# Optimization experiments

Hardware: AMD Instinct MI355X
Metric: run time of the kernel (lower is better)

Reference implementation:

```python
import jax, jax.numpy as jnp
import numpy as np

EMBED_DIM = 64
NUM_CODES = 4096
BETA = 0.25  # commitment_cost


def setup_inputs() -> dict:
    key = jax.random.key(0)
    k1, k2 = jax.random.split(key)
    inputs = jax.random.normal(k1, (512, 8192, 1), dtype=jnp.float32)
    # tf.random_uniform_initializer default range [0, 0.05)
    embeddings = jax.random.uniform(k2, (EMBED_DIM, NUM_CODES), dtype=jnp.float32, minval=0.0, maxval=0.05)
    return {"inputs": inputs, "embeddings": embeddings}


def reference(inputs, embeddings):
    # MuModel.call, training=False (no EMA state updates at inference)
    x = inputs[:, :, 0]                       # [B, T]
    flat = x.reshape(-1, EMBED_DIM)           # [N, D]
    # squared L2 distances to each code: ||z||^2 - 2 z.E + ||e||^2  -> [N, K]
    distances = (
        jnp.sum(flat * flat, axis=1, keepdims=True)
        - 2.0 * (flat @ embeddings)
        + jnp.sum(embeddings * embeddings, axis=0, keepdims=True)
    )
    # tf uses argmax(-distances) == argmin(distances)
    idx = jnp.argmax(-distances, axis=1)      # [N] int
    # one-hot @ embeddings.T is just a gather of code vectors
    quantized = jnp.take(embeddings.T, idx, axis=0)   # [N, D]
    quantized = quantized.reshape(x.shape)            # [B, T]
    commitment_loss = BETA * jnp.mean((jax.lax.stop_gradient(quantized) - x) ** 2)
    quantized = x + jax.lax.stop_gradient(quantized - x)  # straight-through
    out = quantized[..., None]                # [B, T, 1]
    return (out, commitment_loss, idx)
```

## Files before the change

kernel.cpp:

```cpp
#include <hip/hip_runtime.h>
#include <float.h>

#define EMBED   64
#define CODES   4096
#define NROWS   65536
#define NELEM   4194304
#define BR      128
#define CCH     128
#define NCH     32
#define CUNITS  2048
#define NTILE   128

typedef __attribute__((ext_vector_type(8)))  short bf16x8;
typedef __attribute__((ext_vector_type(16))) float f32x16;

__device__ inline unsigned short f2bf(float f) {
    unsigned u = __float_as_uint(f);
    u += 0x7fff + ((u >> 16) & 1);
    return (unsigned short)(u >> 16);
}
__device__ inline float bf2f(unsigned short h) {
    return __uint_as_float(((unsigned)h) << 16);
}

__global__ void vq_setup(const float* __restrict__ E, float* __restrict__ cbuf,
                         double* __restrict__ accum, bf16x8* __restrict__ packed,
                         float* __restrict__ ET) {
    const int b = blockIdx.x, t = threadIdx.x;
    if (b < 16) {
        int j = b * 256 + t;
        float v = E[j];
        float s = __fmul_rn(v, v);
        for (int i = 1; i < EMBED; ++i) {
            v = E[(size_t)i * CODES + j];
            s = __fadd_rn(s, __fmul_rn(v, v));
        }
        cbuf[j] = s;
        if (j == 0) *accum = 0.0;
    } else if (b < 144) {
        int id = (b - 16) * 256 + t;
        int lam = id & 63, kk = (id >> 6) & 3, g = id >> 8;
        int n  = g * 32 + (lam & 31);
        int kb = kk * 16 + (lam >> 5) * 8;
        bf16x8 vh, vl;
#pragma unroll
        for (int j = 0; j < 8; ++j) {
            float e = E[(size_t)(kb + j) * CODES + n];
            unsigned short hi = f2bf(e);
            vh[j] = (short)hi;
            vl[j] = (short)f2bf(e - bf2f(hi));
        }
        packed[((g * 4 + kk) * 2 + 0) * 64 + lam] = vh;
        packed[((g * 4 + kk) * 2 + 1) * 64 + lam] = vl;
    } else {
        int id = (b - 144) * 256 + t;
        int j = id >> 4, i0 = (id & 15) * 4;
        float4 v;
        v.x = E[(size_t)(i0 + 0) * CODES + j];
        v.y = E[(size_t)(i0 + 1) * CODES + j];
        v.z = E[(size_t)(i0 + 2) * CODES + j];
        v.w = E[(size_t)(i0 + 3) * CODES + j];
        *(float4*)(ET + (size_t)j * EMBED + i0) = v;
    }
}

template <bool PRE>
__global__ __launch_bounds__(256, 2)
void vq_main(const float* __restrict__ X, const float* __restrict__ E,
             const float* __restrict__ cbuf, const bf16x8* __restrict__ packed,
             const float* __restrict__ ET, double* __restrict__ accum,
             float* __restrict__ out) {
    __shared__ bf16x8 lbuf[2][CUNITS];

    const int t  = threadIdx.x;
    const int l  = t & 63, wv = t >> 6;
    const int m  = l & 31, h  = l >> 5;
    const int row0 = blockIdx.x * BR;

    bf16x8 ah[4], al[4];
    float sqreg;
    {
        const float* xrow = X + (size_t)(row0 + wv * 32 + m) * EMBED;
        float sq = 0.f;
#pragma unroll
        for (int kk = 0; kk < 4; ++kk) {
            int kb = kk * 16 + h * 8;
            float4 v0 = *(const float4*)(xrow + kb);
            float4 v1 = *(const float4*)(xrow + kb + 4);
            float xv[8] = {v0.x, v0.y, v0.z, v0.w, v1.x, v1.y, v1.z, v1.w};
#pragma unroll
            for (int j = 0; j < 8; ++j) {
                sq = fmaf(xv[j], xv[j], sq);
                unsigned short hi = f2bf(xv[j]);
                float r = xv[j] - bf2f(hi);
                ah[kk][j] = (short)hi;
                al[kk][j] = (short)f2bf(r);
            }
        }
        sq += __shfl_xor(sq, 32, 64);
        sqreg = sq;
    }

    float M1[16], M2[16];
#pragma unroll
    for (int e = 0; e < 16; ++e) { M1[e] = -FLT_MAX; M2[e] = -FLT_MAX; }

    auto epi = [&](const f32x16& a, int g) {
        unsigned gu = (unsigned)g;
#pragma unroll
        for (int e = 0; e < 16; ++e) {
            float ap = __uint_as_float((__float_as_uint(a[e]) & 0xFFFFFF80u) | gu);
            float m1o = M1[e];
            M1[e] = fmaxf(m1o, ap);
            M2[e] = __builtin_amdgcn_fmed3f(m1o, M2[e], ap);
        }
    };

    if constexpr (PRE) {
        auto stage = [&](int ch, int buf) {
#pragma unroll
            for (int q = 0; q < 8; ++q) {
                const bf16x8* gp = packed + (size_t)ch * CUNITS + q * 256 + t;
                bf16x8* lp = &lbuf[buf][q * 256 + wv * 64];
                __builtin_amdgcn_global_load_lds(
                    (const __attribute__((address_space(1))) void*)gp,
                    (__attribute__((address_space(3))) void*)lp, 16, 0, 0);
            }
        };

        f32x16 pA, pB; int pGA = 0, pGB = 0;
#pragma unroll
        for (int e = 0; e < 16; ++e) { pA[e] = -FLT_MAX; pB[e] = -FLT_MAX; }

        const int ch0 = blockIdx.x & (NCH - 1);
        stage(ch0, 0);
        __syncthreads();

        int b = 0;
#pragma unroll 1
        for (int cc = 0; cc < NCH; ++cc) {
            int ch = ch0 + cc; if (ch >= NCH) ch -= NCH;
            if (cc + 1 < NCH) { int cn = ch + 1; if (cn >= NCH) cn -= NCH; stage(cn, b ^ 1); }
            const bf16x8* lb = lbuf[b];
#pragma unroll
            for (int pp = 0; pp < 2; ++pp) {
                const int tl0 = pp * 2, tl1 = tl0 + 1;
                const int g0 = ch * 4 + tl0, g1 = ch * 4 + tl1;
                bf16x8 B0[8], B1[8];
#pragma unroll
                for (int kk = 0; kk < 4; ++kk) {
                    B0[kk * 2]     = lb[tl0 * 512 + kk * 128 + l];
                    B0[kk * 2 + 1] = lb[tl0 * 512 + kk * 128 + 64 + l];
                    B1[kk * 2]     = lb[tl1 * 512 + kk * 128 + l];
                    B1[kk * 2 + 1] = lb[tl1 * 512 + kk * 128 + 64 + l];
                }
                float nc0 = -0.5f * cbuf[g0 * 32 + m];
                float nc1 = -0.5f * cbuf[g1 * 32 + m];
                epi(pA, pGA);
                epi(pB, pGB);
                f32x16 a0, a1;
#pragma unroll
                for (int e = 0; e < 16; ++e) { a0[e] = nc0; a1[e] = nc1; }
#pragma unroll
                for (int kk = 0; kk < 4; ++kk) {
                    a0 = __builtin_amdgcn_mfma_f32_32x32x16_bf16(ah[kk], B0[kk * 2],     a0, 0, 0, 0);
                    a1 = __builtin_amdgcn_mfma_f32_32x32x16_bf16(ah[kk], B1[kk * 2],     a1, 0, 0, 0);
                    a0 = __builtin_amdgcn_mfma_f32_32x32x16_bf16(ah[kk], B0[kk * 2 + 1], a0, 0, 0, 0);
                    a1 = __builtin_amdgcn_mfma_f32_32x32x16_bf16(ah[kk], B1[kk * 2 + 1], a1, 0, 0, 0);
                    a0 = __builtin_amdgcn_mfma_f32_32x32x16_bf16(al[kk], B0[kk * 2],     a0, 0, 0, 0);
                    a1 = __builtin_amdgcn_mfma_f32_32x32x16_bf16(al[kk], B1[kk * 2],     a1, 0, 0, 0);
                }
                pA = a0; pB = a1; pGA = g0; pGB = g1;
            }
            __syncthreads();
            b ^= 1;
        }
        epi(pA, pGA);
        epi(pB, pGB);
    } else {
#pragma unroll 1
        for (int g = 0; g < NTILE; ++g) {
            bf16x8 B[8];
            int n = g * 32 + m;
#pragma unroll
            for (int kk = 0; kk < 4; ++kk) {
                const float* ec = E + (size_t)(kk * 16 + h * 8) * CODES + n;
                bf16x8 vh, vl;
#pragma unroll
                for (int j = 0; j < 8; ++j) {
                    float e = ec[(size_t)j * CODES];
                    unsigned short hi = f2bf(e);
                    vh[j] = (short)hi;
                    vl[j] = (short)f2bf(e - bf2f(hi));
                }
                B[kk * 2] = vh; B[kk * 2 + 1] = vl;
            }
            float nc = -0.5f * cbuf[g * 32 + m];
            f32x16 acc;
#pragma unroll
            for (int e = 0; e < 16; ++e) acc[e] = nc;
#pragma unroll
            for (int kk = 0; kk < 4; ++kk) {
                acc = __builtin_amdgcn_mfma_f32_32x32x16_bf16(ah[kk], B[kk * 2],     acc, 0, 0, 0);
                acc = __builtin_amdgcn_mfma_f32_32x32x16_bf16(ah[kk], B[kk * 2 + 1], acc, 0, 0, 0);
                acc = __builtin_amdgcn_mfma_f32_32x32x16_bf16(al[kk], B[kk * 2],     acc, 0, 0, 0);
            }
            epi(acc, g);
        }
        __syncthreads();
    }

    float* rowm1  = (float*)&lbuf[0][0];
    float* rowsq  = rowm1 + BR;
    int*   rowidx = (int*)(rowsq + BR);
    int*   rowflg = rowidx + BR;
    float* fredv  = (float*)(rowflg + BR);
    int*   fredi  = (int*)(fredv + 256);

    int I1[16];
#pragma unroll
    for (int e = 0; e < 16; ++e)
        I1[e] = (int)(((__float_as_uint(M1[e]) & 0x7Fu) << 5) | (unsigned)m);
#pragma unroll
    for (int d = 1; d < 32; d <<= 1) {
#pragma unroll
        for (int e = 0; e < 16; ++e) {
            float oM1 = __shfl_xor(M1[e], d, 64);
            float oM2 = __shfl_xor(M2[e], d, 64);
            int   oI  = __shfl_xor(I1[e], d, 64);
            float lo  = fminf(M1[e], oM1);
            M2[e] = fmaxf(lo, fmaxf(M2[e], oM2));
            bool c = oM1 > M1[e];
            I1[e] = c ? oI : I1[e];
            M1[e] = c ? oM1 : M1[e];
        }
    }
    if (h == 0) rowsq[wv * 32 + m] = sqreg;
#pragma unroll
    for (int e = 0; e < 16; ++e) {
        int r = (e & 3) + 8 * (e >> 2) + 4 * h;
        if (m == r) {
            rowm1[wv * 32 + r]  = __uint_as_float(__float_as_uint(M1[e]) & 0xFFFFFF80u);
            rowidx[wv * 32 + r] = I1[e];
            rowflg[wv * 32 + r] = (2.f * (M1[e] - M2[e]) < 2e-4f) ? 1 : 0;
        }
    }
    __syncthreads();

#pragma unroll 1
    for (int r = 0; r < BR; ++r) {
        if (rowflg[r] == 0) continue;
        const float* xr = X + (size_t)(row0 + r) * EMBED;
        float racc[8];
#pragma unroll
        for (int jq = 0; jq < 8; ++jq) racc[jq] = __fmul_rn(xr[jq], xr[jq]);
#pragma unroll
        for (int i = 8; i < 64; i += 8)
#pragma unroll
            for (int jq = 0; jq < 8; ++jq)
                racc[jq] = __fadd_rn(racc[jq], __fmul_rn(xr[i + jq], xr[i + jq]));
        float A = __fadd_rn(
            __fadd_rn(__fadd_rn(racc[0], racc[1]), __fadd_rn(racc[2], racc[3])),
            __fadd_rn(__fadd_rn(racc[4], racc[5]), __fadd_rn(racc[6], racc[7])));

        float best = FLT_MAX; int bestj = CODES;
#pragma unroll 1
        for (int jj = 0; jj < 16; ++jj) {
            int j = jj * 256 + t;
            float mm = 0.f;
#pragma unroll
            for (int i = 0; i < 64; ++i)
                mm = fmaf(xr[i], E[(size_t)i * CODES + j], mm);
            float d = __fadd_rn(__fsub_rn(A, __fmul_rn(2.f, mm)), cbuf[j]);
            if (d < best || (d == best && j < bestj)) { best = d; bestj = j; }
        }
        fredv[t] = best; fredi[t] = bestj;
        __syncthreads();
        if (t == 0) {
            float B = fredv[0]; int BI = fredi[0];
            for (int c2 = 1; c2 < 256; ++c2) {
                float dc = fredv[c2]; int jc = fredi[c2];
                if (dc < B || (dc == B && jc < BI)) { B = dc; BI = jc; }
            }
            rowidx[r] = BI;
        }
        __syncthreads();
    }

    if (t < BR) out[(size_t)NELEM + 1 + row0 + t] = (float)rowidx[t];
    if (t == 0) {
        float bs = 0.f;
        for (int r = 0; r < BR; ++r) bs += rowsq[r] - 2.f * rowm1[r];
        atomicAdd(accum, (double)bs);
    }
    {
        int r = t >> 1, i0 = (t & 1) * 32;
        int j = rowidx[r];
        float* dst = out + (size_t)(row0 + r) * EMBED + i0;
        if constexpr (PRE) {
            const float* src = ET + (size_t)j * EMBED + i0;
#pragma unroll
            for (int g = 0; g < 8; ++g)
                *(float4*)(dst + g * 4) = *(const float4*)(src + g * 4);
        } else {
#pragma unroll
            for (int g = 0; g < 8; ++g) {
                float4 v;
                v.x = E[(size_t)(i0 + g * 4 + 0) * CODES + j];
                v.y = E[(size_t)(i0 + g * 4 + 1) * CODES + j];
                v.z = E[(size_t)(i0 + g * 4 + 2) * CODES + j];
                v.w = E[(size_t)(i0 + g * 4 + 3) * CODES + j];
                *(float4*)(dst + g * 4) = v;
            }
        }
    }
}

__global__ void vq_finalize(const double* __restrict__ accum, float* __restrict__ out) {
    out[NELEM] = (float)(0.25 * (*accum) / (double)NELEM);
}

extern "C" void kernel_launch(void* const* d_in, const int* in_sizes, int n_in,
                              void* d_out, int out_size, void* d_ws, size_t ws_size,
                              hipStream_t stream) {
    const float* X = (const float*)d_in[0];
    const float* E = (const float*)d_in[1];
    float* out = (float*)d_out;
    float*  cbuf   = (float*)d_ws;
    double* accum  = (double*)((char*)d_ws + 16384);
    bf16x8* packed = (bf16x8*)((char*)d_ws + 32768);
    float*  ET     = (float*)((char*)d_ws + 32768 + 1048576);
    const size_t need = 32768 + 1048576 + 1048576;
    const bool pre = (ws_size >= need);

    vq_setup<<<pre ? 400 : 16, 256, 0, stream>>>(E, cbuf, accum, packed, ET);
    if (pre)
        vq_main<true><<<NROWS / BR, 256, 0, stream>>>(X, E, cbuf, packed, ET, accum, out);
    else
        vq_main<false><<<NROWS / BR, 256, 0, stream>>>(X, E, cbuf, packed, ET, accum, out);
    vq_finalize<<<1, 1, 0, stream>>>(accum, out);
}
```

Baseline: 264.2 us.

## Split codebook across wave pairs so each wave reuses B tiles over two row tiles

Each wave now holds two 32-row A tiles and handles half of the codebook, instead of one row tile against the full codebook. Every B fragment read from LDS therefore feeds two MFMAs, which halves LDS traffic per MFMA. The per-half argmax candidates are merged through shared memory, and s_setprio is raised around the MFMA bursts. The fallback rescoring path now reads the transposed codebook contiguously. The trade-off is more registers from the doubled A fragments and accumulators, and the software-pipelined epilogue is gone, so the epilogue no longer overlaps with the MFMAs.

```diff
diff --git a/kernel.cpp b/kernel.cpp
--- a/kernel.cpp
+++ b/kernel.cpp
@@ -6,9 +6,7 @@
 #define NROWS   65536
 #define NELEM   4194304
 #define BR      128
-#define CCH     128
-#define NCH     32
-#define CUNITS  2048
+#define NSTEP   32
 #define NTILE   128
 
 typedef __attribute__((ext_vector_type(8)))  short bf16x8;
@@ -64,23 +62,35 @@
     }
 }
 
+#define EPI(a, g, rt) do {                                                     \
+    unsigned gu_ = (unsigned)(g);                                              \
+_Pragma("unroll")                                                              \
+    for (int e = 0; e < 16; ++e) {                                             \
+        float ap_ = __uint_as_float((__float_as_uint((a)[e]) & 0xFFFFFF80u) | gu_); \
+        float m1o_ = M1[rt][e];                                                \
+        M1[rt][e] = fmaxf(m1o_, ap_);                                          \
+        M2[rt][e] = __builtin_amdgcn_fmed3f(m1o_, M2[rt][e], ap_);             \
+    } } while (0)
+
 template <bool PRE>
 __global__ __launch_bounds__(256, 2)
 void vq_main(const float* __restrict__ X, const float* __restrict__ E,
              const float* __restrict__ cbuf, const bf16x8* __restrict__ packed,
              const float* __restrict__ ET, double* __restrict__ accum,
              float* __restrict__ out) {
-    __shared__ bf16x8 lbuf[2][CUNITS];
+    __shared__ bf16x8 lbuf[2][2048];
 
     const int t  = threadIdx.x;
     const int l  = t & 63, wv = t >> 6;
     const int m  = l & 31, h  = l >> 5;
+    const int rg = wv >> 1, ch = wv & 1;
     const int row0 = blockIdx.x * BR;
 
-    bf16x8 ah[4], al[4];
-    float sqreg;
-    {
-        const float* xrow = X + (size_t)(row0 + wv * 32 + m) * EMBED;
+    bf16x8 ah[2][4], al[2][4];
+    float sqv[2];
+#pragma unroll
+    for (int rt = 0; rt < 2; ++rt) {
+        const float* xrow = X + (size_t)(row0 + rg * 64 + rt * 32 + m) * EMBED;
         float sq = 0.f;
 #pragma unroll
         for (int kk = 0; kk < 4; ++kk) {
@@ -93,34 +103,28 @@
                 sq = fmaf(xv[j], xv[j], sq);
                 unsigned short hi = f2bf(xv[j]);
                 float r = xv[j] - bf2f(hi);
-                ah[kk][j] = (short)hi;
-                al[kk][j] = (short)f2bf(r);
+                ah[rt][kk][j] = (short)hi;
+                al[rt][kk][j] = (short)f2bf(r);
             }
         }
         sq += __shfl_xor(sq, 32, 64);
-        sqreg = sq;
-    }
-
-    float M1[16], M2[16];
-#pragma unroll
-    for (int e = 0; e < 16; ++e) { M1[e] = -FLT_MAX; M2[e] = -FLT_MAX; }
-
-    auto epi = [&](const f32x16& a, int g) {
-        unsigned gu = (unsigned)g;
-#pragma unroll
-        for (int e = 0; e < 16; ++e) {
-            float ap = __uint_as_float((__float_as_uint(a[e]) & 0xFFFFFF80u) | gu);
-            float m1o = M1[e];
-            M1[e] = fmaxf(m1o, ap);
-            M2[e] = __builtin_amdgcn_fmed3f(m1o, M2[e], ap);
-        }
-    };
+        sqv[rt] = sq;
+    }
+
+    float M1[2][16], M2[2][16];
+#pragma unroll
+    for (int rt = 0; rt < 2; ++rt)
+#pragma unroll
+        for (int e = 0; e < 16; ++e) { M1[rt][e] = -FLT_MAX; M2[rt][e] = -FLT_MAX; }
 
     if constexpr (PRE) {
-        auto stage = [&](int ch, int buf) {
+        auto stage = [&](int s, int buf) {
 #pragma unroll
             for (int q = 0; q < 8; ++q) {
-                const bf16x8* gp = packed + (size_t)ch * CUNITS + q * 256 + t;
+                int id = q * 256 + t;
+                int hh = id >> 10, w = id & 1023;
+                int g  = hh * 64 + s * 2 + (w >> 9);
+                const bf16x8* gp = packed + (size_t)g * 512 + (w & 511);
                 bf16x8* lp = &lbuf[buf][q * 256 + wv * 64];
                 __builtin_amdgcn_global_load_lds(
                     (const __attribute__((address_space(1))) void*)gp,
@@ -128,60 +132,70 @@
             }
         };
 
-        f32x16 pA, pB; int pGA = 0, pGB = 0;
-#pragma unroll
-        for (int e = 0; e < 16; ++e) { pA[e] = -FLT_MAX; pB[e] = -FLT_MAX; }
-
-        const int ch0 = blockIdx.x & (NCH - 1);
-        stage(ch0, 0);
+        const int s0 = blockIdx.x & (NSTEP - 1);
+        stage(s0, 0);
         __syncthreads();
 
         int b = 0;
 #pragma unroll 1
-        for (int cc = 0; cc < NCH; ++cc) {
-            int ch = ch0 + cc; if (ch >= NCH) ch -= NCH;
-            if (cc + 1 < NCH) { int cn = ch + 1; if (cn >= NCH) cn -= NCH; stage(cn, b ^ 1); }
-            const bf16x8* lb = lbuf[b];
-#pragma unroll
-            for (int pp = 0; pp < 2; ++pp) {
-                const int tl0 = pp * 2, tl1 = tl0 + 1;
-                const int g0 = ch * 4 + tl0, g1 = ch * 4 + tl1;
-                bf16x8 B0[8], B1[8];
-#pragma unroll
-                for (int kk = 0; kk < 4; ++kk) {
-                    B0[kk * 2]     = lb[tl0 * 512 + kk * 128 + l];
-                    B0[kk * 2 + 1] = lb[tl0 * 512 + kk * 128 + 64 + l];
-                    B1[kk * 2]     = lb[tl1 * 512 + kk * 128 + l];
-                    B1[kk * 2 + 1] = lb[tl1 * 512 + kk * 128 + 64 + l];
-                }
-                float nc0 = -0.5f * cbuf[g0 * 32 + m];
-                float nc1 = -0.5f * cbuf[g1 * 32 + m];
-                epi(pA, pGA);
-                epi(pB, pGB);
-                f32x16 a0, a1;
-#pragma unroll
-                for (int e = 0; e < 16; ++e) { a0[e] = nc0; a1[e] = nc1; }
-#pragma unroll
-                for (int kk = 0; kk < 4; ++kk) {
-                    a0 = __builtin_amdgcn_mfma_f32_32x32x16_bf16(ah[kk], B0[kk * 2],     a0, 0, 0, 0);
-                    a1 = __builtin_amdgcn_mfma_f32_32x32x16_bf16(ah[kk], B1[kk * 2],     a1, 0, 0, 0);
-                    a0 = __builtin_amdgcn_mfma_f32_32x32x16_bf16(ah[kk], B0[kk * 2 + 1], a0, 0, 0, 0);
-                    a1 = __builtin_amdgcn_mfma_f32_32x32x16_bf16(ah[kk], B1[kk * 2 + 1], a1, 0, 0, 0);
-                    a0 = __builtin_amdgcn_mfma_f32_32x32x16_bf16(al[kk], B0[kk * 2],     a0, 0, 0, 0);
-                    a1 = __builtin_amdgcn_mfma_f32_32x32x16_bf16(al[kk], B1[kk * 2],     a1, 0, 0, 0);
-                }
-                pA = a0; pB = a1; pGA = g0; pGB = g1;
-            }
+        for (int ss = 0; ss < NSTEP; ++ss) {
+            int s = s0 + ss; if (s >= NSTEP) s -= NSTEP;
+            if (ss + 1 < NSTEP) { int sn = s + 1; if (sn >= NSTEP) sn -= NSTEP; stage(sn, b ^ 1); }
+            const bf16x8* lb = &lbuf[b][ch * 1024];
+            const int g0 = ch * 64 + s * 2;
+            float nc0 = -0.5f * cbuf[g0 * 32 + m];
+            float nc1 = -0.5f * cbuf[g0 * 32 + 32 + m];
+
+            bf16x8 B0[8], B1[8];
+#pragma unroll
+            for (int kk = 0; kk < 4; ++kk) {
+                B0[kk * 2]     = lb[kk * 128 + l];
+                B0[kk * 2 + 1] = lb[kk * 128 + 64 + l];
+                B1[kk * 2]     = lb[512 + kk * 128 + l];
+                B1[kk * 2 + 1] = lb[512 + kk * 128 + 64 + l];
+            }
+
+            f32x16 a0, a1;
+#pragma unroll
+            for (int e = 0; e < 16; ++e) { a0[e] = nc0; a1[e] = nc0; }
+            __builtin_amdgcn_s_setprio(1);
+#pragma unroll
+            for (int kk = 0; kk < 4; ++kk) {
+                a0 = __builtin_amdgcn_mfma_f32_32x32x16_bf16(ah[0][kk], B0[kk * 2],     a0, 0, 0, 0);
+                a1 = __builtin_amdgcn_mfma_f32_32x32x16_bf16(ah[1][kk], B0[kk * 2],     a1, 0, 0, 0);
+                a0 = __builtin_amdgcn_mfma_f32_32x32x16_bf16(ah[0][kk], B0[kk * 2 + 1], a0, 0, 0, 0);
+                a1 = __builtin_amdgcn_mfma_f32_32x32x16_bf16(ah[1][kk], B0[kk * 2 + 1], a1, 0, 0, 0);
+                a0 = __builtin_amdgcn_mfma_f32_32x32x16_bf16(al[0][kk], B0[kk * 2],     a0, 0, 0, 0);
+                a1 = __builtin_amdgcn_mfma_f32_32x32x16_bf16(al[1][kk], B0[kk * 2],     a1, 0, 0, 0);
+            }
+            __builtin_amdgcn_s_setprio(0);
+            EPI(a0, g0, 0);
+            EPI(a1, g0, 1);
+
+#pragma unroll
+            for (int e = 0; e < 16; ++e) { a0[e] = nc1; a1[e] = nc1; }
+            __builtin_amdgcn_s_setprio(1);
+#pragma unroll
+            for (int kk = 0; kk < 4; ++kk) {
+                a0 = __builtin_amdgcn_mfma_f32_32x32x16_bf16(ah[0][kk], B1[kk * 2],     a0, 0, 0, 0);
+                a1 = __builtin_amdgcn_mfma_f32_32x32x16_bf16(ah[1][kk], B1[kk * 2],     a1, 0, 0, 0);
+                a0 = __builtin_amdgcn_mfma_f32_32x32x16_bf16(ah[0][kk], B1[kk * 2 + 1], a0, 0, 0, 0);
+                a1 = __builtin_amdgcn_mfma_f32_32x32x16_bf16(ah[1][kk], B1[kk * 2 + 1], a1, 0, 0, 0);
+                a0 = __builtin_amdgcn_mfma_f32_32x32x16_bf16(al[0][kk], B1[kk * 2],     a0, 0, 0, 0);
+                a1 = __builtin_amdgcn_mfma_f32_32x32x16_bf16(al[1][kk], B1[kk * 2],     a1, 0, 0, 0);
+            }
+            __builtin_amdgcn_s_setprio(0);
+            EPI(a0, g0 + 1, 0);
+            EPI(a1, g0 + 1, 1);
+
             __syncthreads();
             b ^= 1;
         }
-        epi(pA, pGA);
-        epi(pB, pGB);
     } else {
 #pragma unroll 1
-        for (int g = 0; g < NTILE; ++g) {
+        for (int gg = ch * 64; gg < ch * 64 + 64; ++gg) {
             bf16x8 B[8];
-            int n = g * 32 + m;
+            int n = gg * 32 + m;
 #pragma unroll
             for (int kk = 0; kk < 4; ++kk) {
                 const float* ec = E + (size_t)(kk * 16 + h * 8) * CODES + n;
@@ -195,55 +209,85 @@
                 }
                 B[kk * 2] = vh; B[kk * 2 + 1] = vl;
             }
-            float nc = -0.5f * cbuf[g * 32 + m];
-            f32x16 acc;
-#pragma unroll
-            for (int e = 0; e < 16; ++e) acc[e] = nc;
-#pragma unroll
-            for (int kk = 0; kk < 4; ++kk) {
-                acc = __builtin_amdgcn_mfma_f32_32x32x16_bf16(ah[kk], B[kk * 2],     acc, 0, 0, 0);
-                acc = __builtin_amdgcn_mfma_f32_32x32x16_bf16(ah[kk], B[kk * 2 + 1], acc, 0, 0, 0);
-                acc = __builtin_amdgcn_mfma_f32_32x32x16_bf16(al[kk], B[kk * 2],     acc, 0, 0, 0);
-            }
-            epi(acc, g);
+            float nc = -0.5f * cbuf[gg * 32 + m];
+            f32x16 a0, a1;
+#pragma unroll
+            for (int e = 0; e < 16; ++e) { a0[e] = nc; a1[e] = nc; }
+#pragma unroll
+            for (int kk = 0; kk < 4; ++kk) {
+                a0 = __builtin_amdgcn_mfma_f32_32x32x16_bf16(ah[0][kk], B[kk * 2],     a0, 0, 0, 0);
+                a1 = __builtin_amdgcn_mfma_f32_32x32x16_bf16(ah[1][kk], B[kk * 2],     a1, 0, 0, 0);
+                a0 = __builtin_amdgcn_mfma_f32_32x32x16_bf16(ah[0][kk], B[kk * 2 + 1], a0, 0, 0, 0);
+                a1 = __builtin_amdgcn_mfma_f32_32x32x16_bf16(ah[1][kk], B[kk * 2 + 1], a1, 0, 0, 0);
+                a0 = __builtin_amdgcn_mfma_f32_32x32x16_bf16(al[0][kk], B[kk * 2],     a0, 0, 0, 0);
+                a1 = __builtin_amdgcn_mfma_f32_32x32x16_bf16(al[1][kk], B[kk * 2],     a1, 0, 0, 0);
+            }
+            EPI(a0, gg, 0);
+            EPI(a1, gg, 1);
         }
         __syncthreads();
     }
 
-    float* rowm1  = (float*)&lbuf[0][0];
+    float* candM1 = (float*)&lbuf[0][0];
+    float* candM2 = candM1 + 256;
+    int*   candI  = (int*)(candM2 + 256);
+    float* rowm1  = (float*)(candI + 256);
     float* rowsq  = rowm1 + BR;
     int*   rowidx = (int*)(rowsq + BR);
     int*   rowflg = rowidx + BR;
     float* fredv  = (float*)(rowflg + BR);
     int*   fredi  = (int*)(fredv + 256);
 
-    int I1[16];
-#pragma unroll
-    for (int e = 0; e < 16; ++e)
-        I1[e] = (int)(((__float_as_uint(M1[e]) & 0x7Fu) << 5) | (unsigned)m);
+    int I1[2][16];
+#pragma unroll
+    for (int rt = 0; rt < 2; ++rt)
+#pragma unroll
+        for (int e = 0; e < 16; ++e)
+            I1[rt][e] = (int)(((__float_as_uint(M1[rt][e]) & 0x7Fu) << 5) | (unsigned)m);
 #pragma unroll
     for (int d = 1; d < 32; d <<= 1) {
 #pragma unroll
+        for (int rt = 0; rt < 2; ++rt)
+#pragma unroll
+            for (int e = 0; e < 16; ++e) {
+                float oM1 = __shfl_xor(M1[rt][e], d, 64);
+                float oM2 = __shfl_xor(M2[rt][e], d, 64);
+                int   oI  = __shfl_xor(I1[rt][e], d, 64);
+                float lo  = fminf(M1[rt][e], oM1);
+                M2[rt][e] = fmaxf(lo, fmaxf(M2[rt][e], oM2));
+                bool c = oM1 > M1[rt][e];
+                I1[rt][e] = c ? oI : I1[rt][e];
+                M1[rt][e] = c ? oM1 : M1[rt][e];
+            }
+    }
+#pragma unroll
+    for (int rt = 0; rt < 2; ++rt)
+#pragma unroll
         for (int e = 0; e < 16; ++e) {
-            float oM1 = __shfl_xor(M1[e], d, 64);
-            float oM2 = __shfl_xor(M2[e], d, 64);
-            int   oI  = __shfl_xor(I1[e], d, 64);
-            float lo  = fminf(M1[e], oM1);
-            M2[e] = fmaxf(lo, fmaxf(M2[e], oM2));
-            bool c = oM1 > M1[e];
-            I1[e] = c ? oI : I1[e];
-            M1[e] = c ? oM1 : M1[e];
-        }
-    }
-    if (h == 0) rowsq[wv * 32 + m] = sqreg;
-#pragma unroll
-    for (int e = 0; e < 16; ++e) {
-        int r = (e & 3) + 8 * (e >> 2) + 4 * h;
-        if (m == r) {
-            rowm1[wv * 32 + r]  = __uint_as_float(__float_as_uint(M1[e]) & 0xFFFFFF80u);
-            rowidx[wv * 32 + r] = I1[e];
-            rowflg[wv * 32 + r] = (2.f * (M1[e] - M2[e]) < 2e-4f) ? 1 : 0;
-        }
+            int r = (e & 3) + 8 * (e >> 2) + 4 * h;
+            if (m == r) {
+                int row = rg * 64 + rt * 32 + r;
+                candM1[ch * 128 + row] = M1[rt][e];
+                candM2[ch * 128 + row] = M2[rt][e];
+                candI [ch * 128 + row] = I1[rt][e];
+            }
+        }
+    if (ch == 0 && h == 0) {
+        rowsq[rg * 64 + m]      = sqv[0];
+        rowsq[rg * 64 + 32 + m] = sqv[1];
+    }
+    __syncthreads();
+
+    if (t < BR) {
+        float ca = candM1[t],       cb = candM1[128 + t];
+        float a2 = candM2[t],       b2 = candM2[128 + t];
+        bool take = cb > ca;
+        float mm1 = take ? cb : ca;
+        int   ii  = take ? candI[128 + t] : candI[t];
+        float mm2 = fmaxf(fminf(ca, cb), fmaxf(a2, b2));
+        rowm1[t]  = __uint_as_float(__float_as_uint(mm1) & 0xFFFFFF80u);
+        rowidx[t] = ii;
+        rowflg[t] = (2.f * (mm1 - mm2) < 2e-4f) ? 1 : 0;
     }
     __syncthreads();
 
@@ -268,9 +312,16 @@
         for (int jj = 0; jj < 16; ++jj) {
             int j = jj * 256 + t;
             float mm = 0.f;
-#pragma unroll
-            for (int i = 0; i < 64; ++i)
-                mm = fmaf(xr[i], E[(size_t)i * CODES + j], mm);
+            if constexpr (PRE) {
+                const float* er = ET + (size_t)j * EMBED;
+#pragma unroll
+                for (int i = 0; i < 64; ++i)
+                    mm = fmaf(xr[i], er[i], mm);
+            } else {
+#pragma unroll
+                for (int i = 0; i < 64; ++i)
+                    mm = fmaf(xr[i], E[(size_t)i * CODES + j], mm);
+            }
             float d = __fadd_rn(__fsub_rn(A, __fmul_rn(2.f, mm)), cbuf[j]);
             if (d < best || (d == best && j < bestj)) { best = d; bestj = j; }
         }
```

Measured after the change: 323.0 us. 1.22x slower.

## Triple-buffer codebook staging with finer chunks and LDS-resident code norms

Applied to the files above, without the earlier changes.

The codebook is now staged in 64 smaller chunks through a three-deep LDS ring buffer using async global-to-LDS loads. Explicit vmcnt waits replace the full __syncthreads, so up to two chunks are in flight while the MFMAs run. Code norms are preloaded into LDS instead of read from global memory each tile. The fallback row recheck now reads the transposed codebook contiguously. The trade-off is more barriers per code, since each chunk is half the size, and more LDS use, which may affect the two-blocks-per-CU occupancy.

```diff
diff --git a/kernel.cpp b/kernel.cpp
--- a/kernel.cpp
+++ b/kernel.cpp
@@ -6,9 +6,7 @@
 #define NROWS   65536
 #define NELEM   4194304
 #define BR      128
-#define CCH     128
-#define NCH     32
-#define CUNITS  2048
+#define NCH     64
 #define NTILE   128
 
 typedef __attribute__((ext_vector_type(8)))  short bf16x8;
@@ -70,7 +68,8 @@
              const float* __restrict__ cbuf, const bf16x8* __restrict__ packed,
              const float* __restrict__ ET, double* __restrict__ accum,
              float* __restrict__ out) {
-    __shared__ bf16x8 lbuf[2][CUNITS];
+    __shared__ float  cbuf_lds[CODES];
+    __shared__ bf16x8 lbuf[3][1024];
 
     const int t  = threadIdx.x;
     const int l  = t & 63, wv = t >> 6;
@@ -117,63 +116,82 @@
     };
 
     if constexpr (PRE) {
-        auto stage = [&](int ch, int buf) {
-#pragma unroll
-            for (int q = 0; q < 8; ++q) {
-                const bf16x8* gp = packed + (size_t)ch * CUNITS + q * 256 + t;
-                bf16x8* lp = &lbuf[buf][q * 256 + wv * 64];
+        auto stage = [&](int s, int bi) {
+#pragma unroll
+            for (int q = 0; q < 4; ++q) {
+                const bf16x8* gp = packed + (size_t)s * 1024 + q * 256 + t;
+                bf16x8* lp = &lbuf[bi][q * 256 + wv * 64];
                 __builtin_amdgcn_global_load_lds(
                     (const __attribute__((address_space(1))) void*)gp,
                     (__attribute__((address_space(3))) void*)lp, 16, 0, 0);
             }
         };
 
+#pragma unroll
+        for (int q = 0; q < 4; ++q) {
+            const float* gp = cbuf + (size_t)(q * 256 + t) * 4;
+            char* lp = (char*)cbuf_lds + (size_t)(q * 256 + wv * 64) * 16;
+            __builtin_amdgcn_global_load_lds(
+                (const __attribute__((address_space(1))) void*)gp,
+                (__attribute__((address_space(3))) void*)lp, 16, 0, 0);
+        }
+        const int s0 = blockIdx.x & (NCH - 1);
+        stage(s0, 0);
+        stage((s0 + 1) & (NCH - 1), 1);
+
         f32x16 pA, pB; int pGA = 0, pGB = 0;
 #pragma unroll
         for (int e = 0; e < 16; ++e) { pA[e] = -FLT_MAX; pB[e] = -FLT_MAX; }
 
-        const int ch0 = blockIdx.x & (NCH - 1);
-        stage(ch0, 0);
-        __syncthreads();
-
-        int b = 0;
+        asm volatile("s_waitcnt vmcnt(4)" ::: "memory");
+        __builtin_amdgcn_sched_barrier(0);
+        __builtin_amdgcn_s_barrier();
+        __builtin_amdgcn_sched_barrier(0);
+
+        int bi = 0;
 #pragma unroll 1
         for (int cc = 0; cc < NCH; ++cc) {
-            int ch = ch0 + cc; if (ch >= NCH) ch -= NCH;
-            if (cc + 1 < NCH) { int cn = ch + 1; if (cn >= NCH) cn -= NCH; stage(cn, b ^ 1); }
-            const bf16x8* lb = lbuf[b];
-#pragma unroll
-            for (int pp = 0; pp < 2; ++pp) {
-                const int tl0 = pp * 2, tl1 = tl0 + 1;
-                const int g0 = ch * 4 + tl0, g1 = ch * 4 + tl1;
-                bf16x8 B0[8], B1[8];
-#pragma unroll
-                for (int kk = 0; kk < 4; ++kk) {
-                    B0[kk * 2]     = lb[tl0 * 512 + kk * 128 + l];
-                    B0[kk * 2 + 1] = lb[tl0 * 512 + kk * 128 + 64 + l];
-                    B1[kk * 2]     = lb[tl1 * 512 + kk * 128 + l];
-                    B1[kk * 2 + 1] = lb[tl1 * 512 + kk * 128 + 64 + l];
-                }
-                float nc0 = -0.5f * cbuf[g0 * 32 + m];
-                float nc1 = -0.5f * cbuf[g1 * 32 + m];
-                epi(pA, pGA);
-                epi(pB, pGB);
-                f32x16 a0, a1;
-#pragma unroll
-                for (int e = 0; e < 16; ++e) { a0[e] = nc0; a1[e] = nc1; }
-#pragma unroll
-                for (int kk = 0; kk < 4; ++kk) {
-                    a0 = __builtin_amdgcn_mfma_f32_32x32x16_bf16(ah[kk], B0[kk * 2],     a0, 0, 0, 0);
-                    a1 = __builtin_amdgcn_mfma_f32_32x32x16_bf16(ah[kk], B1[kk * 2],     a1, 0, 0, 0);
-                    a0 = __builtin_amdgcn_mfma_f32_32x32x16_bf16(ah[kk], B0[kk * 2 + 1], a0, 0, 0, 0);
-                    a1 = __builtin_amdgcn_mfma_f32_32x32x16_bf16(ah[kk], B1[kk * 2 + 1], a1, 0, 0, 0);
-                    a0 = __builtin_amdgcn_mfma_f32_32x32x16_bf16(al[kk], B0[kk * 2],     a0, 0, 0, 0);
-                    a1 = __builtin_amdgcn_mfma_f32_32x32x16_bf16(al[kk], B1[kk * 2],     a1, 0, 0, 0);
-                }
-                pA = a0; pB = a1; pGA = g0; pGB = g1;
-            }
-            __syncthreads();
-            b ^= 1;
+            int s = s0 + cc; if (s >= NCH) s -= NCH;
+            const bf16x8* lb = lbuf[bi];
+            const int g0 = 2 * s, g1 = g0 + 1;
+            float nc0 = -0.5f * cbuf_lds[g0 * 32 + m];
+            float nc1 = -0.5f * cbuf_lds[g1 * 32 + m];
+            bf16x8 B0[8], B1[8];
+#pragma unroll
+            for (int kk = 0; kk < 4; ++kk) {
+                B0[kk * 2]     = lb[kk * 128 + l];
+                B0[kk * 2 + 1] = lb[kk * 128 + 64 + l];
+                B1[kk * 2]     = lb[512 + kk * 128 + l];
+                B1[kk * 2 + 1] = lb[512 + kk * 128 + 64 + l];
+            }
+            epi(pA, pGA);
+            epi(pB, pGB);
+            f32x16 a0, a1;
+#pragma unroll
+            for (int e = 0; e < 16; ++e) { a0[e] = nc0; a1[e] = nc1; }
+#pragma unroll
+            for (int kk = 0; kk < 4; ++kk) {
+                a0 = __builtin_amdgcn_mfma_f32_32x32x16_bf16(ah[kk], B0[kk * 2],     a0, 0, 0, 0);
+                a1 = __builtin_amdgcn_mfma_f32_32x32x16_bf16(ah[kk], B1[kk * 2],     a1, 0, 0, 0);
+                a0 = __builtin_amdgcn_mfma_f32_32x32x16_bf16(ah[kk], B0[kk * 2 + 1], a0, 0, 0, 0);
+                a1 = __builtin_amdgcn_mfma_f32_32x32x16_bf16(ah[kk], B1[kk * 2 + 1], a1, 0, 0, 0);
+                a0 = __builtin_amdgcn_mfma_f32_32x32x16_bf16(al[kk], B0[kk * 2],     a0, 0, 0, 0);
+                a1 = __builtin_amdgcn_mfma_f32_32x32x16_bf16(al[kk], B1[kk * 2],     a1, 0, 0, 0);
+            }
+            pA = a0; pB = a1; pGA = g0; pGB = g1;
+
+            if (cc < NCH - 2) {
+                int sn = s + 2; if (sn >= NCH) sn -= NCH;
+                int sb = bi + 2; if (sb >= 3) sb -= 3;
+                stage(sn, sb);
+                asm volatile("s_waitcnt vmcnt(4)" ::: "memory");
+            } else {
+                asm volatile("s_waitcnt vmcnt(0)" ::: "memory");
+            }
+            __builtin_amdgcn_sched_barrier(0);
+            __builtin_amdgcn_s_barrier();
+            __builtin_amdgcn_sched_barrier(0);
+            if (++bi == 3) bi = 0;
         }
         epi(pA, pGA);
         epi(pB, pGB);
@@ -268,9 +286,16 @@
         for (int jj = 0; jj < 16; ++jj) {
             int j = jj * 256 + t;
             float mm = 0.f;
-#pragma unroll
-            for (int i = 0; i < 64; ++i)
-                mm = fmaf(xr[i], E[(size_t)i * CODES + j], mm);
+            if constexpr (PRE) {
+                const float* er = ET + (size_t)j * EMBED;
+#pragma unroll
+                for (int i = 0; i < 64; ++i)
+                    mm = fmaf(xr[i], er[i], mm);
+            } else {
+#pragma unroll
+                for (int i = 0; i < 64; ++i)
+                    mm = fmaf(xr[i], E[(size_t)i * CODES + j], mm);
+            }
             float d = __fadd_rn(__fsub_rn(A, __fmul_rn(2.f, mm)), cbuf[j]);
             if (d < best || (d == best && j < bestj)) { best = d; bestj = j; }
         }
```

Result: slower. 334.0 us (+26.4%).

## Split codebook across wave pairs and read packed codes directly from global

Applied to the files above, without the earlier changes.

Each block now handles 64 rows instead of 128. Two waves share each 32-row group, and each wave scans half of the codebook. The waves read packed bf16 code tiles directly from global or L2 instead of staging them through double-buffered LDS with global_load_lds. Their per-half argmax candidates are merged through small shared arrays. The goal is to drop LDS staging, barriers and the large LDS footprint so occupancy can rise to 4 blocks per SU; the cost is more L2 traffic and a per-lane global load latency that has no explicit prefetch. The tie-fallback path also switches to the transposed codebook for contiguous row reads.

```diff
diff --git a/kernel.cpp b/kernel.cpp
--- a/kernel.cpp
+++ b/kernel.cpp
@@ -5,10 +5,8 @@
 #define CODES   4096
 #define NROWS   65536
 #define NELEM   4194304
-#define BR      128
-#define CCH     128
-#define NCH     32
-#define CUNITS  2048
+#define BR      64
+#define NPAIR   32
 #define NTILE   128
 
 typedef __attribute__((ext_vector_type(8)))  short bf16x8;
@@ -65,22 +63,29 @@
 }
 
 template <bool PRE>
-__global__ __launch_bounds__(256, 2)
+__global__ __launch_bounds__(256, 4)
 void vq_main(const float* __restrict__ X, const float* __restrict__ E,
              const float* __restrict__ cbuf, const bf16x8* __restrict__ packed,
              const float* __restrict__ ET, double* __restrict__ accum,
              float* __restrict__ out) {
-    __shared__ bf16x8 lbuf[2][CUNITS];
+    __shared__ float candM1[2][BR];
+    __shared__ float candM2[2][BR];
+    __shared__ int   candI [2][BR];
+    __shared__ float rowm1[BR], rowsq[BR];
+    __shared__ int   rowidx[BR], rowflg[BR];
+    __shared__ float fredv[256];
+    __shared__ int   fredi[256];
 
     const int t  = threadIdx.x;
     const int l  = t & 63, wv = t >> 6;
     const int m  = l & 31, h  = l >> 5;
+    const int rg = wv >> 1, ch = wv & 1;
     const int row0 = blockIdx.x * BR;
 
     bf16x8 ah[4], al[4];
     float sqreg;
     {
-        const float* xrow = X + (size_t)(row0 + wv * 32 + m) * EMBED;
+        const float* xrow = X + (size_t)(row0 + rg * 32 + m) * EMBED;
         float sq = 0.f;
 #pragma unroll
         for (int kk = 0; kk < 4; ++kk) {
@@ -117,71 +122,50 @@
     };
 
     if constexpr (PRE) {
-        auto stage = [&](int ch, int buf) {
-#pragma unroll
-            for (int q = 0; q < 8; ++q) {
-                const bf16x8* gp = packed + (size_t)ch * CUNITS + q * 256 + t;
-                bf16x8* lp = &lbuf[buf][q * 256 + wv * 64];
-                __builtin_amdgcn_global_load_lds(
-                    (const __attribute__((address_space(1))) void*)gp,
-                    (__attribute__((address_space(3))) void*)lp, 16, 0, 0);
-            }
-        };
-
         f32x16 pA, pB; int pGA = 0, pGB = 0;
 #pragma unroll
         for (int e = 0; e < 16; ++e) { pA[e] = -FLT_MAX; pB[e] = -FLT_MAX; }
 
-        const int ch0 = blockIdx.x & (NCH - 1);
-        stage(ch0, 0);
-        __syncthreads();
-
-        int b = 0;
+        const int p0 = blockIdx.x & (NPAIR - 1);
 #pragma unroll 1
-        for (int cc = 0; cc < NCH; ++cc) {
-            int ch = ch0 + cc; if (ch >= NCH) ch -= NCH;
-            if (cc + 1 < NCH) { int cn = ch + 1; if (cn >= NCH) cn -= NCH; stage(cn, b ^ 1); }
-            const bf16x8* lb = lbuf[b];
-#pragma unroll
-            for (int pp = 0; pp < 2; ++pp) {
-                const int tl0 = pp * 2, tl1 = tl0 + 1;
-                const int g0 = ch * 4 + tl0, g1 = ch * 4 + tl1;
-                bf16x8 B0[8], B1[8];
-#pragma unroll
-                for (int kk = 0; kk < 4; ++kk) {
-                    B0[kk * 2]     = lb[tl0 * 512 + kk * 128 + l];
-                    B0[kk * 2 + 1] = lb[tl0 * 512 + kk * 128 + 64 + l];
-                    B1[kk * 2]     = lb[tl1 * 512 + kk * 128 + l];
-                    B1[kk * 2 + 1] = lb[tl1 * 512 + kk * 128 + 64 + l];
-                }
-                float nc0 = -0.5f * cbuf[g0 * 32 + m];
-                float nc1 = -0.5f * cbuf[g1 * 32 + m];
-                epi(pA, pGA);
-                epi(pB, pGB);
-                f32x16 a0, a1;
-#pragma unroll
-                for (int e = 0; e < 16; ++e) { a0[e] = nc0; a1[e] = nc1; }
-#pragma unroll
-                for (int kk = 0; kk < 4; ++kk) {
-                    a0 = __builtin_amdgcn_mfma_f32_32x32x16_bf16(ah[kk], B0[kk * 2],     a0, 0, 0, 0);
-                    a1 = __builtin_amdgcn_mfma_f32_32x32x16_bf16(ah[kk], B1[kk * 2],     a1, 0, 0, 0);
-                    a0 = __builtin_amdgcn_mfma_f32_32x32x16_bf16(ah[kk], B0[kk * 2 + 1], a0, 0, 0, 0);
-                    a1 = __builtin_amdgcn_mfma_f32_32x32x16_bf16(ah[kk], B1[kk * 2 + 1], a1, 0, 0, 0);
-                    a0 = __builtin_amdgcn_mfma_f32_32x32x16_bf16(al[kk], B0[kk * 2],     a0, 0, 0, 0);
-                    a1 = __builtin_amdgcn_mfma_f32_32x32x16_bf16(al[kk], B1[kk * 2],     a1, 0, 0, 0);
-                }
-                pA = a0; pB = a1; pGA = g0; pGB = g1;
-            }
-            __syncthreads();
-            b ^= 1;
+        for (int pp = 0; pp < NPAIR; ++pp) {
+            int p = p0 + pp; if (p >= NPAIR) p -= NPAIR;
+            const int g0 = ch * 64 + 2 * p, g1 = g0 + 1;
+            const bf16x8* q0 = packed + (size_t)g0 * 512;
+            const bf16x8* q1 = packed + (size_t)g1 * 512;
+            float nc0 = -0.5f * cbuf[g0 * 32 + m];
+            float nc1 = -0.5f * cbuf[g1 * 32 + m];
+            bf16x8 B0[8], B1[8];
+#pragma unroll
+            for (int kk = 0; kk < 4; ++kk) {
+                B0[kk * 2]     = q0[kk * 128 + l];
+                B0[kk * 2 + 1] = q0[kk * 128 + 64 + l];
+                B1[kk * 2]     = q1[kk * 128 + l];
+                B1[kk * 2 + 1] = q1[kk * 128 + 64 + l];
+            }
+            epi(pA, pGA);
+            epi(pB, pGB);
+            f32x16 a0, a1;
+#pragma unroll
+            for (int e = 0; e < 16; ++e) { a0[e] = nc0; a1[e] = nc1; }
+#pragma unroll
+            for (int kk = 0; kk < 4; ++kk) {
+                a0 = __builtin_amdgcn_mfma_f32_32x32x16_bf16(ah[kk], B0[kk * 2],     a0, 0, 0, 0);
+                a1 = __builtin_amdgcn_mfma_f32_32x32x16_bf16(ah[kk], B1[kk * 2],     a1, 0, 0, 0);
+                a0 = __builtin_amdgcn_mfma_f32_32x32x16_bf16(ah[kk], B0[kk * 2 + 1], a0, 0, 0, 0);
+                a1 = __builtin_amdgcn_mfma_f32_32x32x16_bf16(ah[kk], B1[kk * 2 + 1], a1, 0, 0, 0);
+                a0 = __builtin_amdgcn_mfma_f32_32x32x16_bf16(al[kk], B0[kk * 2],     a0, 0, 0, 0);
+                a1 = __builtin_amdgcn_mfma_f32_32x32x16_bf16(al[kk], B1[kk * 2],     a1, 0, 0, 0);
+            }
+            pA = a0; pB = a1; pGA = g0; pGB = g1;
         }
         epi(pA, pGA);
         epi(pB, pGB);
     } else {
 #pragma unroll 1
-        for (int g = 0; g < NTILE; ++g) {
+        for (int gg = ch * 64; gg < ch * 64 + 64; ++gg) {
             bf16x8 B[8];
-            int n = g * 32 + m;
+            int n = gg * 32 + m;
 #pragma unroll
             for (int kk = 0; kk < 4; ++kk) {
                 const float* ec = E + (size_t)(kk * 16 + h * 8) * CODES + n;
@@ -195,7 +179,7 @@
                 }
                 B[kk * 2] = vh; B[kk * 2 + 1] = vl;
             }
-            float nc = -0.5f * cbuf[g * 32 + m];
+            float nc = -0.5f * cbuf[gg * 32 + m];
             f32x16 acc;
 #pragma unroll
             for (int e = 0; e < 16; ++e) acc[e] = nc;
@@ -205,17 +189,9 @@
                 acc = __builtin_amdgcn_mfma_f32_32x32x16_bf16(ah[kk], B[kk * 2 + 1], acc, 0, 0, 0);
                 acc = __builtin_amdgcn_mfma_f32_32x32x16_bf16(al[kk], B[kk * 2],     acc, 0, 0, 0);
             }
-            epi(acc, g);
-        }
-        __syncthreads();
-    }
-
-    float* rowm1  = (float*)&lbuf[0][0];
-    float* rowsq  = rowm1 + BR;
-    int*   rowidx = (int*)(rowsq + BR);
-    int*   rowflg = rowidx + BR;
-    float* fredv  = (float*)(rowflg + BR);
-    int*   fredi  = (int*)(fredv + 256);
+            epi(acc, gg);
+        }
+    }
 
     int I1[16];
 #pragma unroll
@@ -235,15 +211,28 @@
             M1[e] = c ? oM1 : M1[e];
         }
     }
-    if (h == 0) rowsq[wv * 32 + m] = sqreg;
 #pragma unroll
     for (int e = 0; e < 16; ++e) {
         int r = (e & 3) + 8 * (e >> 2) + 4 * h;
         if (m == r) {
-            rowm1[wv * 32 + r]  = __uint_as_float(__float_as_uint(M1[e]) & 0xFFFFFF80u);
-            rowidx[wv * 32 + r] = I1[e];
-            rowflg[wv * 32 + r] = (2.f * (M1[e] - M2[e]) < 2e-4f) ? 1 : 0;
-        }
+            candM1[ch][rg * 32 + r] = M1[e];
+            candM2[ch][rg * 32 + r] = M2[e];
+            candI [ch][rg * 32 + r] = I1[e];
+        }
+    }
+    if (ch == 0 && h == 0) rowsq[rg * 32 + m] = sqreg;
+    __syncthreads();
+
+    if (t < BR) {
+        float ca = candM1[0][t], cb = candM1[1][t];
+        float a2 = candM2[0][t], b2 = candM2[1][t];
+        bool take = cb > ca;
+        float mm1 = take ? cb : ca;
+        int   ii  = take ? candI[1][t] : candI[0][t];
+        float mm2 = fmaxf(fminf(ca, cb), fmaxf(a2, b2));
+        rowm1[t]  = __uint_as_float(__float_as_uint(mm1) & 0xFFFFFF80u);
+        rowidx[t] = ii;
+        rowflg[t] = (2.f * (mm1 - mm2) < 2e-4f) ? 1 : 0;
     }
     __syncthreads();
 
@@ -268,9 +257,16 @@
         for (int jj = 0; jj < 16; ++jj) {
             int j = jj * 256 + t;
             float mm = 0.f;
-#pragma unroll
-            for (int i = 0; i < 64; ++i)
-                mm = fmaf(xr[i], E[(size_t)i * CODES + j], mm);
+            if constexpr (PRE) {
+                const float* er = ET + (size_t)j * EMBED;
+#pragma unroll
+                for (int i = 0; i < 64; ++i)
+                    mm = fmaf(xr[i], er[i], mm);
+            } else {
+#pragma unroll
+                for (int i = 0; i < 64; ++i)
+                    mm = fmaf(xr[i], E[(size_t)i * CODES + j], mm);
+            }
             float d = __fadd_rn(__fsub_rn(A, __fmul_rn(2.f, mm)), cbuf[j]);
             if (d < best || (d == best && j < bestj)) { best = d; bestj = j; }
         }
@@ -294,17 +290,17 @@
         atomicAdd(accum, (double)bs);
     }
     {
-        int r = t >> 1, i0 = (t & 1) * 32;
+        int r = t >> 2, i0 = (t & 3) * 16;
         int j = rowidx[r];
         float* dst = out + (size_t)(row0 + r) * EMBED + i0;
         if constexpr (PRE) {
             const float* src = ET + (size_t)j * EMBED + i0;
 #pragma unroll
-            for (int g = 0; g < 8; ++g)
+            for (int g = 0; g < 4; ++g)
                 *(float4*)(dst + g * 4) = *(const float4*)(src + g * 4);
         } else {
 #pragma unroll
-            for (int g = 0; g < 8; ++g) {
+            for (int g = 0; g < 4; ++g) {
                 float4 v;
                 v.x = E[(size_t)(i0 + g * 4 + 0) * CODES + j];
                 v.y = E[(size_t)(i0 + g * 4 + 1) * CODES + j];
```

New measurement: 487.6 us. 84.6% more time.
